# Performance work log

Hardware: AMD Instinct MI355X
Metric: run time of the kernel (lower is better)

The kernel has to match this reference:

```python
import jax, jax.numpy as jnp
import numpy as np

WS = 8          # attention window size
NUM_HEADS = 4
PATCH_RATIO = 2 # ratio between consecutive pyramid levels
SCALES = 3


def _rel_idx(ws):
    ch = np.arange(ws)
    coords = np.stack(np.meshgrid(ch, ch, indexing='ij')).reshape(2, -1)
    rel = (coords[:, :, None] - coords[:, None, :]).transpose(1, 2, 0)
    rel[:, :, 0] += ws - 1
    rel[:, :, 1] += ws - 1
    rel[:, :, 0] *= 2 * ws - 1
    return jnp.asarray(rel.sum(-1))  # [ws*ws, ws*ws] int

REL_IDX = _rel_idx(WS)


def win_part(x, ws):
    B, H, W, C = x.shape
    x = x.reshape(B, H // ws, ws, W // ws, ws, C).transpose(0, 1, 3, 2, 4, 5)
    return x.reshape(-1, ws, ws, C)


def win_rev(w, ws, B, H, W):
    C = w.shape[-1]
    x = w.reshape(B, H // ws, W // ws, ws, ws, C).transpose(0, 1, 3, 2, 4, 5)
    return x.reshape(B, H, W, C)


def cross_attn(xw, yw, mw, qw, qb, kw, kb, vw, vb, pw, pb, table):
    # xw, yw: [Bn, N, C]; mw: [Bn, N] overexposure mask
    Bn, N, C = xw.shape
    hd = C // NUM_HEADS
    scale = hd ** -0.5
    q = (xw @ qw.T + qb).reshape(Bn, N, NUM_HEADS, hd).transpose(0, 2, 1, 3) * scale
    k = (yw @ kw.T + kb).reshape(Bn, N, NUM_HEADS, hd).transpose(0, 2, 1, 3)
    v = (yw @ vw.T + vb).reshape(Bn, N, NUM_HEADS, hd).transpose(0, 2, 1, 3)
    attn = jnp.einsum('bhnd,bhmd->bhnm', q, k)
    mask_attn = mw[:, None, :] * mw[:, :, None]          # [Bn, N, N]
    attn = attn * mask_attn[:, None]                     # multiplicative exposure mask
    bias = table[REL_IDX]                                # [N, N, heads]
    attn = attn + bias.transpose(2, 0, 1)[None]
    attn = jax.nn.softmax(attn, axis=-1)
    out = jnp.einsum('bhnm,bhmd->bhnd', attn, v).transpose(0, 2, 1, 3).reshape(Bn, N, C)
    out = out @ pw.T + pb
    return out, attn


def align_level(x, y, params):
    # x, y: [B, H, W, C]; shift_size = 0 (module default)
    B, H, W, C = x.shape
    mask = jnp.where(x > 0.95, 0.0, 1.0).mean(-1, keepdims=True)  # [B,H,W,1]
    x = x * mask
    xw = win_part(x, WS).reshape(-1, WS * WS, C)
    yw = win_part(y, WS).reshape(-1, WS * WS, C)
    mw = win_part(mask, WS).reshape(-1, WS * WS)
    out, attn = cross_attn(xw, yw, mw, *params)
    out = win_rev(out.reshape(-1, WS, WS, C), WS, B, H, W)
    return out, attn


def atttransfer(ta, att, pr):
    # ta: [B, H, W, C] at finer level; att: [nW, heads, WS^2, WS^2] from coarser level
    B, H, W, C = ta.shape
    ws = WS * pr
    w = win_part(ta, ws)                                  # [nW, ws, ws, C]
    nW = w.shape[0]
    w = w.reshape(nW, WS, pr, WS, pr, C).transpose(0, 1, 3, 2, 4, 5)
    w = w.reshape(nW, WS * WS, pr * pr * C)
    out = att.mean(axis=1) @ w                            # [nW, WS^2, pr^2*C]
    out = out.reshape(nW, WS, WS, pr, pr, C).transpose(0, 1, 3, 2, 4, 5).reshape(nW, ws, ws, C)
    return win_rev(out, ws, B, H, W)


def conv3(x, w, b):
    y = jax.lax.conv_general_dilated(x, w, (1, 1), 'SAME',
                                     dimension_numbers=('NCHW', 'OIHW', 'NCHW'))
    return y + b[None, :, None, None]


def lrelu(x):
    return jax.nn.leaky_relu(x, 0.1)


def _forward(ref1, ref2, ref3, ta1, ta2, ta3, q_w, q_b, k_w, k_b, v_w, v_b,
             p_w, p_b, bias_table, fc_w, fc_b):
    refs = [ref1, ref2, ref3]
    tas = [ta1, ta2, ta3]
    upsample_feat = None
    last_att = None
    feat = None
    for i in range(SCALES, 0, -1):
        j = i - 1
        ref = refs[j].transpose(0, 2, 3, 1)   # NCHW -> NHWC
        ta = tas[j].transpose(0, 2, 3, 1)
        params = (q_w[j], q_b[j], k_w[j], k_b[j], v_w[j], v_b[j],
                  p_w[j], p_b[j], bias_table[j])
        aligned, att = align_level(ref, ta, params)
        feat = aligned.transpose(0, 3, 1, 2)  # NHWC -> NCHW
        if i < SCALES:
            atrans = atttransfer(ta, last_att, PATCH_RATIO).transpose(0, 3, 1, 2)
            feat = conv3(jnp.concatenate([feat, upsample_feat, atrans], axis=1),
                         fc_w[j], fc_b[j])
        if i > 1:
            feat = lrelu(feat)
            B, C, Hh, Ww = feat.shape
            upsample_feat = jax.image.resize(feat, (B, C, Hh * 2, Ww * 2), method='bilinear')
        last_att = att
    return lrelu(feat)


def setup_inputs() -> dict:
    key = jax.random.key(0)
    ks = jax.random.split(key, 20)
    B, C = 4, 64
    d = {}
    d['ref1'] = jax.random.normal(ks[0], (B, C, 256, 256), jnp.float32)
    d['ref2'] = jax.random.normal(ks[1], (B, C, 128, 128), jnp.float32)
    d['ref3'] = jax.random.normal(ks[2], (B, C, 64, 64), jnp.float32)
    d['ta1'] = jax.random.normal(ks[3], (B, C, 256, 256), jnp.float32)
    d['ta2'] = jax.random.normal(ks[4], (B, C, 128, 128), jnp.float32)
    d['ta3'] = jax.random.normal(ks[5], (B, C, 64, 64), jnp.float32)
    d['q_w'] = jax.random.normal(ks[6], (3, C, C), jnp.float32) * 0.02
    d['q_b'] = jax.random.normal(ks[7], (3, C), jnp.float32) * 0.02
    d['k_w'] = jax.random.normal(ks[8], (3, C, C), jnp.float32) * 0.02
    d['k_b'] = jax.random.normal(ks[9], (3, C), jnp.float32) * 0.02
    d['v_w'] = jax.random.normal(ks[10], (3, C, C), jnp.float32) * 0.02
    d['v_b'] = jax.random.normal(ks[11], (3, C), jnp.float32) * 0.02
    d['p_w'] = jax.random.normal(ks[12], (3, C, C), jnp.float32) * 0.02
    d['p_b'] = jax.random.normal(ks[13], (3, C), jnp.float32) * 0.02
    d['bias_table'] = jax.random.normal(ks[14], (3, (2 * WS - 1) ** 2, NUM_HEADS), jnp.float32) * 0.02
    d['fc_w'] = jax.random.normal(ks[15], (2, C, 3 * C, 3, 3), jnp.float32) * 0.02
    d['fc_b'] = jax.random.normal(ks[16], (2, C), jnp.float32) * 0.02
    return d


def reference(ref1, ref2, ref3, ta1, ta2, ta3, q_w, q_b, k_w, k_b, v_w, v_b,
              p_w, p_b, bias_table, fc_w, fc_b):
    return _forward(ref1, ref2, ref3, ta1, ta2, ta3, q_w, q_b, k_w, k_b,
                    v_w, v_b, p_w, p_b, bias_table, fc_w, fc_b)
```

## Files before the change

kernel.cpp:

```cpp
#include <hip/hip_runtime.h>
#include <hip/hip_bf16.h>
#include <math.h>

#define LRELU(v) ((v) >= 0.f ? (v) : 0.1f * (v))
#define LOG2E 1.4426950408889634f

typedef __attribute__((ext_vector_type(8))) short short8;
typedef __attribute__((ext_vector_type(4))) float f32x4;

#define MFMA16 __builtin_amdgcn_mfma_f32_16x16x32_bf16

__device__ __forceinline__ float loadf(const float* p) { return *p; }
__device__ __forceinline__ float loadf(const __hip_bfloat16* p) { return __bfloat162float(*p); }
__device__ __forceinline__ short f2bfbits(float f) {
    __hip_bfloat16 h = __float2bfloat16(f);
    return *reinterpret_cast<short*>(&h);
}
__device__ __forceinline__ float bits2f(unsigned short u) {
    union { unsigned int i; float f; } x; x.i = ((unsigned int)u) << 16; return x.f;
}
__device__ __forceinline__ float lo2f(unsigned int v) {
    union { unsigned int i; float f; } x; x.i = v << 16; return x.f;
}
__device__ __forceinline__ float hi2f(unsigned int v) {
    union { unsigned int i; float f; } x; x.i = v & 0xFFFF0000u; return x.f;
}

__global__ __launch_bounds__(256) void nhwc_kernel(const float* __restrict__ ref,
                                                   const float* __restrict__ ta,
                                                   __hip_bfloat16* __restrict__ refn,
                                                   __hip_bfloat16* __restrict__ tan,
                                                   float* __restrict__ maskp,
                                                   int H, int HW) {
    __shared__ float S[2][64][67];
    const int tid = threadIdx.x;
    const int tile = blockIdx.x;
    const int b = blockIdx.y;
    const int tpr = H >> 6;
    const int y = tile / tpr;
    const int x0 = (tile - y * tpr) << 6;
    const size_t ibase = (size_t)b * 64 * HW + (size_t)y * H + x0;

    for (int r = tid; r < 8192; r += 256) {
        int which = r >> 12;
        int c = (r >> 6) & 63;
        int x = r & 63;
        S[which][c][x] = (which ? ta : ref)[ibase + (size_t)c * HW + x];
    }
    __syncthreads();
    if (tid < 64) {
        float s = 0.f;
#pragma unroll
        for (int c = 0; c < 64; ++c) s += (S[0][c][tid] > 0.95f) ? 0.f : 1.f;
        maskp[(size_t)b * HW + (size_t)y * H + x0 + tid] = s * (1.f / 64.f);
    }
    const size_t obase = ((size_t)b * HW + (size_t)y * H + x0) * 64;
    for (int r = tid; r < 8192; r += 256) {
        int which = r >> 12;
        int x = (r >> 6) & 63;
        int c = r & 63;
        (which ? tan : refn)[obase + (size_t)x * 64 + c] = __float2bfloat16(S[which][c][x]);
    }
}

template <bool HASATT>
__global__ __launch_bounds__(256, 4) void fused_attn_kernel(
    const __hip_bfloat16* __restrict__ refn,
    const __hip_bfloat16* __restrict__ tan,
    const float* __restrict__ maskp,
    const __hip_bfloat16* __restrict__ WQ,
    const __hip_bfloat16* __restrict__ WK,
    const __hip_bfloat16* __restrict__ WV,
    const __hip_bfloat16* __restrict__ WPp,
    const float* __restrict__ qb, const float* __restrict__ kb,
    const float* __restrict__ vb, const float* __restrict__ pb,
    const float* __restrict__ btab,
    __hip_bfloat16* __restrict__ aligned,
    __hip_bfloat16* __restrict__ attm,
    int H, int nWx, int nWin)
{
    __shared__ __align__(16) unsigned short PP[64 * 72];
    __shared__ __align__(16) unsigned short KH[64 * 72];
    __shared__ __align__(16) unsigned short VT[64 * 72];
    __shared__ __align__(8) unsigned short BLB[900];
    __shared__ float MSK[64];

    const int HW = H * H;
    const int win = blockIdx.x;
    const int bb = blockIdx.y;
    const int wy = win / nWx, wx = win - wy * nWx;
    const int y0 = wy * 8, x0 = wx * 8;
    const int tid = threadIdx.x;
    const int w = __builtin_amdgcn_readfirstlane(tid >> 6);
    const int l = tid & 63;
    const int lq = l >> 4, lm = l & 15;

    for (int r = tid; r < 900; r += 256)
        BLB[r] = (unsigned short)f2bfbits(btab[r] * LOG2E);
    if (tid < 64)
        MSK[tid] = maskp[(size_t)bb * HW + (size_t)(y0 + (tid >> 3)) * H + x0 + (tid & 7)];

    const int tokr = 16 * w + lm;
    const size_t prow = ((size_t)bb * HW
                         + (size_t)(y0 + (tokr >> 3)) * H + (x0 + (tokr & 7))) * 64;
    const unsigned short* xp = (const unsigned short*)refn + prow;
    const unsigned short* yp = (const unsigned short*)tan + prow;

    f32x4 aq[4], ak[4], av[4];
#pragma unroll
    for (int nt = 0; nt < 4; ++nt) {
        aq[nt] = (f32x4){0.f, 0.f, 0.f, 0.f};
        ak[nt] = (f32x4){0.f, 0.f, 0.f, 0.f};
        av[nt] = (f32x4){0.f, 0.f, 0.f, 0.f};
    }

#pragma unroll
    for (int stage = 0; stage < 2; ++stage) {
        const int cio = stage * 32 + lq * 8;
        short8 xa = *reinterpret_cast<const short8*>(xp + cio);
        short8 ya = *reinterpret_cast<const short8*>(yp + cio);
#pragma unroll
        for (int nt = 0; nt < 4; ++nt) {
            const int co = nt * 16 + lm;
            short8 bq = *reinterpret_cast<const short8*>(WQ + co * 64 + cio);
            aq[nt] = MFMA16(xa, bq, aq[nt], 0, 0, 0);
            short8 bk = *reinterpret_cast<const short8*>(WK + co * 64 + cio);
            ak[nt] = MFMA16(ya, bk, ak[nt], 0, 0, 0);
            short8 bv8 = *reinterpret_cast<const short8*>(WV + co * 64 + cio);
            av[nt] = MFMA16(ya, bv8, av[nt], 0, 0, 0);
        }
    }

#pragma unroll
    for (int nt = 0; nt < 4; ++nt) {
        const int co = nt * 16 + lm;
        const float kbv = kb[co], vbv = vb[co];
#pragma unroll
        for (int r = 0; r < 4; ++r) {
            const int tr = 16 * w + lq * 4 + r;
            const int pr = 16 * (2 * (tr >> 5) + ((tr >> 2) & 1))
                         + 4 * ((tr >> 3) & 3) + (tr & 3);
            KH[pr * 72 + co] = (unsigned short)f2bfbits(ak[nt][r] + kbv);
            VT[co * 72 + tr] = (unsigned short)f2bfbits(av[nt][r] + vbv);
        }
    }
    {
        float mq_r[4];
#pragma unroll
        for (int r = 0; r < 4; ++r) mq_r[r] = MSK[16 * w + lq * 4 + r];
#pragma unroll
        for (int nt = 0; nt < 4; ++nt) {
            const float qbv = qb[nt * 16 + lm];
#pragma unroll
            for (int r = 0; r < 4; ++r)
                PP[(16 * w + lq * 4 + r) * 72 + nt * 16 + lm] =
                    (unsigned short)f2bfbits((aq[nt][r] * mq_r[r] + qbv) * 0.25f);
        }
    }
    __syncthreads();

    const short8 z8 = (short8){0, 0, 0, 0, 0, 0, 0, 0};
    const f32x4 zf = (f32x4){0.f, 0.f, 0.f, 0.f};
    short8 qfrag[4];
#pragma unroll
    for (int h = 0; h < 4; ++h)
        qfrag[h] = (lq < 2)
            ? *reinterpret_cast<const short8*>(&PP[(16 * w + lm) * 72 + 16 * h + lq * 8])
            : z8;

    const float mql = MSK[16 * w + lm] * LOG2E;
    const int qt = 16 * w + lm;
    const int qi = qt >> 3, qj = qt & 7;
    float m2[4][4];
    int bofs[4][4];
    int ktab[4][4];
#pragma unroll
    for (int nt = 0; nt < 4; ++nt)
#pragma unroll
        for (int r = 0; r < 4; ++r) {
            int kt = (nt >> 1) * 32 + lq * 8 + (nt & 1) * 4 + r;
            ktab[nt][r] = kt;
            m2[nt][r] = mql * MSK[kt];
            bofs[nt][r] = ((qi - (kt >> 3) + 7) * 15 + (qj - (kt & 7) + 7)) * 4;
        }

    float attAcc[HASATT ? 4 : 1][HASATT ? 4 : 1];
    if constexpr (HASATT) {
#pragma unroll
        for (int nt = 0; nt < 4; ++nt)
#pragma unroll
            for (int r = 0; r < 4; ++r) attAcc[nt][r] = 0.f;
    }
    f32x4 oacc[4];

#pragma unroll
    for (int hp = 0; hp < 2; ++hp) {
        unsigned int blv[4][4];
#pragma unroll
        for (int nt = 0; nt < 4; ++nt)
#pragma unroll
            for (int r = 0; r < 4; ++r)
                blv[nt][r] = *reinterpret_cast<const unsigned int*>(
                                 &BLB[bofs[nt][r] + hp * 2]);

        f32x4 s[2][4];
#pragma unroll
        for (int u = 0; u < 2; ++u) {
            const int h = hp * 2 + u;
#pragma unroll
            for (int nt = 0; nt < 4; ++nt) {
                short8 kf = (lq < 2)
                    ? *reinterpret_cast<const short8*>(
                          &KH[(nt * 16 + lm) * 72 + 16 * h + lq * 8])
                    : z8;
                s[u][nt] = MFMA16(kf, qfrag[h], zf, 0, 0, 0);
            }
        }

        float p[2][4][4];
#pragma unroll
        for (int u = 0; u < 2; ++u)
#pragma unroll
            for (int nt = 0; nt < 4; ++nt)
#pragma unroll
                for (int r = 0; r < 4; ++r) {
                    float bias = u ? hi2f(blv[nt][r]) : lo2f(blv[nt][r]);
                    p[u][nt][r] = fmaf(s[u][nt][r], m2[nt][r], bias);
                }

        float inv[2];
#pragma unroll
        for (int u = 0; u < 2; ++u) {
            float a0 = fmaxf(p[u][0][0], p[u][0][1]);
            float a1 = fmaxf(p[u][0][2], p[u][0][3]);
            float a2 = fmaxf(p[u][1][0], p[u][1][1]);
            float a3 = fmaxf(p[u][1][2], p[u][1][3]);
            float a4 = fmaxf(p[u][2][0], p[u][2][1]);
            float a5 = fmaxf(p[u][2][2], p[u][2][3]);
            float a6 = fmaxf(p[u][3][0], p[u][3][1]);
            float a7 = fmaxf(p[u][3][2], p[u][3][3]);
            float b0 = fmaxf(a0, a1), b1 = fmaxf(a2, a3);
            float b2 = fmaxf(a4, a5), b3 = fmaxf(a6, a7);
            float m = fmaxf(fmaxf(b0, b1), fmaxf(b2, b3));
            m = fmaxf(m, __shfl_xor(m, 16));
            m = fmaxf(m, __shfl_xor(m, 32));
            float sm = 0.f;
#pragma unroll
            for (int nt = 0; nt < 4; ++nt)
#pragma unroll
                for (int r = 0; r < 4; ++r) {
                    p[u][nt][r] = exp2f(p[u][nt][r] - m);
                    sm += p[u][nt][r];
                }
            sm += __shfl_xor(sm, 16);
            sm += __shfl_xor(sm, 32);
            inv[u] = 1.f / sm;
        }

        if constexpr (HASATT) {
#pragma unroll
            for (int u = 0; u < 2; ++u) {
                const float sc = 0.25f * inv[u];
#pragma unroll
                for (int nt = 0; nt < 4; ++nt)
#pragma unroll
                    for (int r = 0; r < 4; ++r)
                        attAcc[nt][r] = fmaf(sc, p[u][nt][r], attAcc[nt][r]);
            }
        }

#pragma unroll
        for (int u = 0; u < 2; ++u) {
            const int h = hp * 2 + u;
            short8 pb0, pb1;
#pragma unroll
            for (int j = 0; j < 8; ++j) {
                pb0[j] = f2bfbits(p[u][(j >> 2)][j & 3]);
                pb1[j] = f2bfbits(p[u][2 + (j >> 2)][j & 3]);
            }
            short8 vt0 = *reinterpret_cast<const short8*>(&VT[(16 * h + lm) * 72 + lq * 8]);
            short8 vt1 = *reinterpret_cast<const short8*>(&VT[(16 * h + lm) * 72 + 32 + lq * 8]);
            f32x4 o = MFMA16(vt0, pb0, zf, 0, 0, 0);
            o = MFMA16(vt1, pb1, o, 0, 0, 0);
            oacc[h][0] = o[0] * inv[u]; oacc[h][1] = o[1] * inv[u];
            oacc[h][2] = o[2] * inv[u]; oacc[h][3] = o[3] * inv[u];
        }
    }

    if constexpr (HASATT) {
#pragma unroll
        for (int nt = 0; nt < 4; ++nt)
#pragma unroll
            for (int r = 0; r < 4; ++r)
                PP[(16 * w + lm) * 72 + ktab[nt][r]] =
                    (unsigned short)f2bfbits(attAcc[nt][r]);
        const int rr = 16 * w + (l >> 2), cb = (l & 3) * 16;
        short8 a0 = *reinterpret_cast<const short8*>(&PP[rr * 72 + cb]);
        short8 a1 = *reinterpret_cast<const short8*>(&PP[rr * 72 + cb + 8]);
        unsigned short* gp = (unsigned short*)attm
            + ((size_t)bb * nWin + win) * 4096 + (size_t)rr * 64 + cb;
        *reinterpret_cast<short8*>(gp) = a0;
        *reinterpret_cast<short8*>(gp + 8) = a1;
    }

    short8 oa0, oa1;
#pragma unroll
    for (int j = 0; j < 8; ++j) {
        oa0[j] = f2bfbits(oacc[(j >> 2)][j & 3]);
        oa1[j] = f2bfbits(oacc[2 + (j >> 2)][j & 3]);
    }
    f32x4 eo[4];
#pragma unroll
    for (int nt = 0; nt < 4; ++nt) {
        const int co = nt * 16 + lm;
        short8 wb0 = *reinterpret_cast<const short8*>(WPp + co * 64 + lq * 8);
        short8 wb1 = *reinterpret_cast<const short8*>(WPp + co * 64 + 32 + lq * 8);
        eo[nt] = MFMA16(oa0, wb0, zf, 0, 0, 0);
        eo[nt] = MFMA16(oa1, wb1, eo[nt], 0, 0, 0);
    }
    const size_t obase = (size_t)bb * HW * 64;
#pragma unroll
    for (int nt = 0; nt < 4; ++nt) {
        float pbv = pb[nt * 16 + lm];
#pragma unroll
        for (int r = 0; r < 4; ++r) {
            int tok = 16 * w + lq * 4 + r;
            aligned[obase + ((size_t)(y0 + (tok >> 3)) * H + (x0 + (tok & 7))) * 64
                    + nt * 16 + lm] = __float2bfloat16(eo[nt][r] + pbv);
        }
    }
}

__global__ __launch_bounds__(256) void wsplit_kernel(const float* __restrict__ qw,
                                                     const float* __restrict__ kw,
                                                     const float* __restrict__ vw,
                                                     const float* __restrict__ pw,
                                                     __hip_bfloat16* __restrict__ dst) {
    int idx = blockIdx.x * 256 + threadIdx.x;
    int e = idx & 4095;
    int mat = (idx >> 12) & 3;
    int j = idx >> 14;
    int co = e >> 6, ci = e & 63;
    int src_ci = ci;
    if (mat == 3)
        src_ci = 16 * (2 * (ci >> 5) + ((ci >> 2) & 1)) + 4 * ((ci >> 3) & 3) + (ci & 3);
    const float* src = (mat == 0 ? qw : mat == 1 ? kw : mat == 2 ? vw : pw) + j * 4096;
    float v = src[co * 64 + src_ci];
    __hip_bfloat16 h = __float2bfloat16(v);
    dst[((size_t)j * 4 + mat) * 8192 + e] = h;
    dst[((size_t)j * 4 + mat) * 8192 + 4096 + e] = __float2bfloat16(v - __bfloat162float(h));
}

#define PSTR 4624
__global__ __launch_bounds__(256) void atttrans_kernel(
    const __hip_bfloat16* __restrict__ tan,
    const __hip_bfloat16* __restrict__ attm,
    __hip_bfloat16* __restrict__ outw,
    int H, int HW, int nWx16)
{
    __shared__ __align__(16) unsigned short AT[4608];
    __shared__ __align__(16) unsigned short VTP[4 * PSTR];

    const int tid = threadIdx.x;
    const int win = blockIdx.x;
    const int b = blockIdx.y;
    const int wh = win / nWx16, ww = win - wh * nWx16;
    const int w = __builtin_amdgcn_readfirstlane(tid >> 6);
    const int l = tid & 63;
    const int lq = l >> 4, lm = l & 15;

    const unsigned short* ap = (const unsigned short*)attm
        + ((size_t)b * nWx16 * nWx16 + win) * 4096;
    for (int s = tid; s < 512; s += 256) {
        short8 v = *reinterpret_cast<const short8*>(ap + s * 8);
        *reinterpret_cast<short8*>(&AT[(s >> 3) * 72 + (s & 7) * 8]) = v;
    }

    {
        const int yy = tid >> 4, xx = tid & 15;
        const int pp = ((yy & 1) << 1) | (xx & 1);
        const int s = ((yy >> 1) << 3) | (xx >> 1);
        const unsigned short* tp = (const unsigned short*)tan
            + ((size_t)b * HW + (size_t)(wh * 16 + yy) * H + (ww * 16 + xx)) * 64;
        unsigned short* vbp = &VTP[pp * PSTR + s];
#pragma unroll
        for (int oct = 0; oct < 8; ++oct) {
            short8 v = *reinterpret_cast<const short8*>(tp + oct * 8);
#pragma unroll
            for (int i = 0; i < 8; ++i) vbp[(oct * 8 + i) * 72] = (unsigned short)v[i];
        }
    }
    __syncthreads();

    f32x4 acc[4][4];
#pragma unroll
    for (int pp = 0; pp < 4; ++pp)
#pragma unroll
        for (int nt = 0; nt < 4; ++nt) acc[pp][nt] = (f32x4){0.f, 0.f, 0.f, 0.f};

#pragma unroll
    for (int kk = 0; kk < 2; ++kk) {
        short8 aA = *reinterpret_cast<const short8*>(
                        &AT[(16 * w + lm) * 72 + kk * 32 + lq * 8]);
#pragma unroll
        for (int pp = 0; pp < 4; ++pp) {
#pragma unroll
            for (int nt = 0; nt < 4; ++nt) {
                short8 bB = *reinterpret_cast<const short8*>(
                    &VTP[pp * PSTR + (nt * 16 + lm) * 72 + kk * 32 + lq * 8]);
                acc[pp][nt] = MFMA16(aA, bB, acc[pp][nt], 0, 0, 0);
            }
        }
    }

#pragma unroll
    for (int pp = 0; pp < 4; ++pp) {
        const int pi = pp >> 1, pj = pp & 1;
#pragma unroll
        for (int r = 0; r < 4; ++r) {
            const int t = 16 * w + lq * 4 + r;
            const int Y = wh * 16 + ((t >> 3) << 1) + pi;
            const int X = ww * 16 + ((t & 7) << 1) + pj;
            __hip_bfloat16* op = outw + ((size_t)b * HW + (size_t)Y * H + X) * 64;
#pragma unroll
            for (int nt = 0; nt < 4; ++nt)
                op[nt * 16 + lm] = __float2bfloat16(acc[pp][nt][r]);
        }
    }
}

__global__ __launch_bounds__(256) void wtrans_kernel(const float* __restrict__ src,
                                                     __hip_bfloat16* __restrict__ WH,
                                                     __hip_bfloat16* __restrict__ WL) {
    int idx = blockIdx.x * 256 + threadIdx.x;
    int j = idx & 7;
    int t1 = idx >> 3;
    int co = t1 & 63;
    int t2 = t1 >> 6;
    int oct = t2 & 3;
    int t3 = t2 >> 2;
    int chunk = t3 % 6;
    int kykx = t3 / 6;
    int ci = chunk * 32 + oct * 8 + j;
    int ky = kykx / 3, kx = kykx % 3;
    float v = src[((co * 192 + ci) * 3 + ky) * 3 + kx];
    __hip_bfloat16 h = __float2bfloat16(v);
    WH[idx] = h;
    WL[idx] = __float2bfloat16(v - __bfloat162float(h));
}

__global__ __launch_bounds__(256) void conv_mfma_kernel(
    const __hip_bfloat16* __restrict__ s0, const __hip_bfloat16* __restrict__ s1,
    const __hip_bfloat16* __restrict__ s2,
    const __hip_bfloat16* __restrict__ WHp,
    const float* __restrict__ bias,
    float* __restrict__ out,
    int H, int HW, int mode)
{
    __shared__ short I[6][66][40];

    const int tid = threadIdx.x;
    const int w   = tid >> 6;
    const int l   = tid & 63;
    const int lq  = l >> 4;
    const int lm  = l & 15;
    const int x0  = blockIdx.x * 64;
    const int y0  = blockIdx.y * 4;
    const size_t zoff = (size_t)blockIdx.z * HW * 64;
    const short8 z8 = (short8){0, 0, 0, 0, 0, 0, 0, 0};

    f32x4 acc[4][4];
#pragma unroll
    for (int mt = 0; mt < 4; ++mt)
#pragma unroll
        for (int nt = 0; nt < 4; ++nt) acc[mt][nt] = (f32x4){0.f, 0.f, 0.f, 0.f};

    const short8* WH8 = reinterpret_cast<const short8*>(WHp);

    short8 st[7];
    const unsigned short* b0 = (const unsigned short*)s0;
    const unsigned short* b1 = (const unsigned short*)s1;
    const unsigned short* b2 = (const unsigned short*)s2;

    auto stage_load = [&](int chunk) {
        const unsigned short* src = (chunk < 2) ? b0 : (chunk < 4) ? b1 : b2;
        const int cib = (chunk & 1) * 32;
#pragma unroll
        for (int s = 0; s < 7; ++s) {
            int slot = tid + (s << 8);
            if (slot < 1584) {
                int oct = slot & 3;
                int xr = slot >> 2;
                int xi = xr % 66;
                int r = xr / 66;
                int gx = x0 - 1 + xi, gy = y0 - 1 + r;
                short8 v = z8;
                if (gx >= 0 && gx < H && gy >= 0 && gy < H)
                    v = *reinterpret_cast<const short8*>(
                            src + zoff + ((size_t)gy * H + gx) * 64 + cib + oct * 8);
                st[s] = v;
            }
        }
    };
    auto stage_write = [&]() {
#pragma unroll
        for (int s = 0; s < 7; ++s) {
            int slot = tid + (s << 8);
            if (slot < 1584) {
                int oct = slot & 3;
                int xr = slot >> 2;
                int xi = xr % 66;
                int r = xr / 66;
                *reinterpret_cast<short8*>(&I[r][xi][oct * 8]) = st[s];
            }
        }
    };

    stage_load(0);
    stage_write();
    __syncthreads();

    for (int chunk = 0; chunk < 6; ++chunk) {
        if (chunk < 5) stage_load(chunk + 1);
#pragma unroll
        for (int kk = 0; kk < 9; ++kk) {
            const int ky = kk / 3, kx = kk % 3;
            const int wbase = ((kk * 6 + chunk) * 4 + lq) * 64 + lm;
            short8 ah[4];
#pragma unroll
            for (int mt = 0; mt < 4; ++mt) ah[mt] = WH8[wbase + mt * 16];
#pragma unroll
            for (int nt = 0; nt < 4; ++nt) {
                short8 bfrag = *reinterpret_cast<const short8*>(
                                   &I[w + ky][nt * 16 + lm + kx][lq * 8]);
#pragma unroll
                for (int mt = 0; mt < 4; ++mt)
                    acc[mt][nt] = MFMA16(ah[mt], bfrag, acc[mt][nt], 0, 0, 0);
            }
        }
        if (chunk < 5) {
            __syncthreads();
            stage_write();
            __syncthreads();
        }
    }

    const int y = y0 + w;
#pragma unroll
    for (int mt = 0; mt < 4; ++mt) {
#pragma unroll
        for (int r = 0; r < 4; ++r) {
            const int co = mt * 16 + lq * 4 + r;
            const float bv = bias[co];
#pragma unroll
            for (int nt = 0; nt < 4; ++nt) {
                float v = acc[mt][nt][r] + bv;
                const int x = x0 + nt * 16 + lm;
                if (mode == 0) {
                    v = LRELU(v);
                    out[zoff + (size_t)co * HW + (size_t)y * H + x] = v;
                } else {
                    out[zoff + ((size_t)y * H + x) * 64 + co] = v;
                }
            }
        }
    }
}

template <typename T>
__global__ __launch_bounds__(256) void upsample_kernel(const T* __restrict__ in,
                                                       __hip_bfloat16* __restrict__ out,
                                                       int Hin, int total) {
    int idx = blockIdx.x * 256 + threadIdx.x;
    if (idx >= total) return;
    int c = idx & 63;
    int r1 = idx >> 6;
    int W2 = Hin * 2;
    int X = r1 % W2;
    int r2 = r1 / W2;
    int Y = r2 % W2;
    int b = r2 / W2;
    int y0 = Y >> 1, x0 = X >> 1;
    int ya = (Y & 1) ? y0 + 1 : y0 - 1;
    int xa = (X & 1) ? x0 + 1 : x0 - 1;
    ya = ya < 0 ? 0 : (ya >= Hin ? Hin - 1 : ya);
    xa = xa < 0 ? 0 : (xa >= Hin ? Hin - 1 : xa);
    const T* p = in + (size_t)b * Hin * Hin * 64;
    float v00 = LRELU(loadf(p + ((size_t)y0 * Hin + x0) * 64 + c));
    float v01 = LRELU(loadf(p + ((size_t)y0 * Hin + xa) * 64 + c));
    float v10 = LRELU(loadf(p + ((size_t)ya * Hin + x0) * 64 + c));
    float v11 = LRELU(loadf(p + ((size_t)ya * Hin + xa) * 64 + c));
    out[idx] = __float2bfloat16(0.5625f * v00 + 0.1875f * (v01 + v10) + 0.0625f * v11);
}

extern "C" void kernel_launch(void* const* d_in, const int* in_sizes, int n_in,
                              void* d_out, int out_size, void* d_ws, size_t ws_size,
                              hipStream_t stream) {
    const float* refs[3] = { (const float*)d_in[0], (const float*)d_in[1], (const float*)d_in[2] };
    const float* tas[3]  = { (const float*)d_in[3], (const float*)d_in[4], (const float*)d_in[5] };
    const float* q_w = (const float*)d_in[6];
    const float* q_b = (const float*)d_in[7];
    const float* k_w = (const float*)d_in[8];
    const float* k_b = (const float*)d_in[9];
    const float* v_w = (const float*)d_in[10];
    const float* v_b = (const float*)d_in[11];
    const float* p_w = (const float*)d_in[12];
    const float* p_b = (const float*)d_in[13];
    const float* btab = (const float*)d_in[14];
    const float* fc_w = (const float*)d_in[15];
    const float* fc_b = (const float*)d_in[16];

    const size_t WBYTES = 4ull * 221184 + 196608;
    const size_t BIG4 = 4ull * 65536 * 64 * 2;
    const size_t NEED4 = WBYTES + 4 * BIG4 + 4ull * 65536 * 4 + 4096;
    const int NB = (ws_size >= NEED4) ? 4 : 1;
    const size_t BIG = (size_t)NB * 65536 * 64 * 2;

    char* p = (char*)d_ws;
    __hip_bfloat16* WH0 = (__hip_bfloat16*)p;  p += 221184;
    __hip_bfloat16* WL0 = (__hip_bfloat16*)p;  p += 221184;
    __hip_bfloat16* WH1 = (__hip_bfloat16*)p;  p += 221184;
    __hip_bfloat16* WL1 = (__hip_bfloat16*)p;  p += 221184;
    __hip_bfloat16* WTA = (__hip_bfloat16*)p;  p += 196608;
    __hip_bfloat16* XRN = (__hip_bfloat16*)p;  p += BIG;
    __hip_bfloat16* XTN = (__hip_bfloat16*)p;  p += BIG;
    __hip_bfloat16* ALIGNED = (__hip_bfloat16*)p;  p += BIG;
    __hip_bfloat16* UPS     = (__hip_bfloat16*)p;  p += BIG;
    float* MASKP = (float*)p;  p += (size_t)NB * 65536 * 4;
    __hip_bfloat16* ATRANS = XRN;
    __hip_bfloat16 *ATTMA, *ATTMB;
    float* FEAT2;
    if (NB == 4) {
        ATTMA = (__hip_bfloat16*)d_out;
        ATTMB = (__hip_bfloat16*)((float*)d_out + 1048576);
        FEAT2 = (float*)d_out + 5242880;
    } else {
        ATTMA = (__hip_bfloat16*)p;  p += (size_t)64 * 4096 * 2;
        ATTMB = (__hip_bfloat16*)p;  p += (size_t)256 * 4096 * 2;
        FEAT2 = (float*)p;           p += (size_t)16384 * 64 * 4;
    }

    wtrans_kernel<<<432, 256, 0, stream>>>(fc_w, WH0, WL0);
    wtrans_kernel<<<432, 256, 0, stream>>>(fc_w + 110592, WH1, WL1);
    wsplit_kernel<<<192, 256, 0, stream>>>(q_w, k_w, v_w, p_w, WTA);

    for (int b0 = 0; b0 < 4; b0 += NB) {
        const float* ref1 = refs[0] + (size_t)b0 * 64 * 65536;
        const float* ta1  = tas[0]  + (size_t)b0 * 64 * 65536;
        const float* ref2 = refs[1] + (size_t)b0 * 64 * 16384;
        const float* ta2  = tas[1]  + (size_t)b0 * 64 * 16384;
        const float* ref3 = refs[2] + (size_t)b0 * 64 * 4096;
        const float* ta3  = tas[2]  + (size_t)b0 * 64 * 4096;

        nhwc_kernel<<<dim3(64, NB), 256, 0, stream>>>(ref3, ta3, XRN, XTN, MASKP, 64, 4096);
        fused_attn_kernel<true><<<dim3(64, NB), 256, 0, stream>>>(
            XRN, XTN, MASKP,
            WTA + (2*4+0)*8192, WTA + (2*4+1)*8192, WTA + (2*4+2)*8192, WTA + (2*4+3)*8192,
            q_b + 2*64, k_b + 2*64, v_b + 2*64, p_b + 2*64,
            btab + 2*900, ALIGNED, ATTMA, 64, 8, 64);
        upsample_kernel<__hip_bfloat16><<<(NB * 64 * 16384) / 256, 256, 0, stream>>>(
            ALIGNED, UPS, 64, NB * 64 * 16384);

        nhwc_kernel<<<dim3(256, NB), 256, 0, stream>>>(ref2, ta2, XRN, XTN, MASKP, 128, 16384);
        fused_attn_kernel<true><<<dim3(256, NB), 256, 0, stream>>>(
            XRN, XTN, MASKP,
            WTA + (1*4+0)*8192, WTA + (1*4+1)*8192, WTA + (1*4+2)*8192, WTA + (1*4+3)*8192,
            q_b + 64, k_b + 64, v_b + 64, p_b + 64,
            btab + 900, ALIGNED, ATTMB, 128, 16, 256);
        atttrans_kernel<<<dim3(64, NB), 256, 0, stream>>>(
            XTN, ATTMA, ATRANS, 128, 16384, 8);
        conv_mfma_kernel<<<dim3(2, 32, NB), 256, 0, stream>>>(
            ALIGNED, UPS, ATRANS, WH1, fc_b + 64, FEAT2, 128, 16384, 1);
        upsample_kernel<float><<<(NB * 64 * 65536) / 256, 256, 0, stream>>>(
            FEAT2, UPS, 128, NB * 64 * 65536);

        nhwc_kernel<<<dim3(1024, NB), 256, 0, stream>>>(ref1, ta1, XRN, XTN, MASKP, 256, 65536);
        fused_attn_kernel<false><<<dim3(1024, NB), 256, 0, stream>>>(
            XRN, XTN, MASKP,
            WTA + 0*8192, WTA + 1*8192, WTA + 2*8192, WTA + 3*8192,
            q_b, k_b, v_b, p_b,
            btab, ALIGNED, nullptr, 256, 32, 1024);
        atttrans_kernel<<<dim3(256, NB), 256, 0, stream>>>(
            XTN, ATTMB, ATRANS, 256, 65536, 16);
        conv_mfma_kernel<<<dim3(4, 64, NB), 256, 0, stream>>>(
            ALIGNED, UPS, ATRANS, WH0, fc_b,
            (float*)d_out + (size_t)b0 * 64 * 65536, 256, 65536, 0);
    }
}
```

Baseline: 411.2 us.

## Load conv input fragments directly from global memory instead of LDS staging

Removes the shared-memory tile, its register-staged double buffering, and the block barriers in the 3x3 conv MFMA kernel. Each lane now reads its B-fragment straight from global memory, with bounds checks for the padding. This drops the LDS traffic and synchronisation. In exchange, each input element is re-fetched up to nine times (3x3 taps) across waves and relies on the caches to absorb it, and global-load latency is no longer hidden by the prefetch pipeline.

```diff
diff --git a/kernel.cpp b/kernel.cpp
--- a/kernel.cpp
+++ b/kernel.cpp
@@ -457,8 +457,6 @@
     float* __restrict__ out,
     int H, int HW, int mode)
 {
-    __shared__ short I[6][66][40];
-
     const int tid = threadIdx.x;
     const int w   = tid >> 6;
     const int l   = tid & 63;
@@ -476,52 +474,13 @@
         for (int nt = 0; nt < 4; ++nt) acc[mt][nt] = (f32x4){0.f, 0.f, 0.f, 0.f};
 
     const short8* WH8 = reinterpret_cast<const short8*>(WHp);
-
-    short8 st[7];
-    const unsigned short* b0 = (const unsigned short*)s0;
-    const unsigned short* b1 = (const unsigned short*)s1;
-    const unsigned short* b2 = (const unsigned short*)s2;
-
-    auto stage_load = [&](int chunk) {
-        const unsigned short* src = (chunk < 2) ? b0 : (chunk < 4) ? b1 : b2;
-        const int cib = (chunk & 1) * 32;
-#pragma unroll
-        for (int s = 0; s < 7; ++s) {
-            int slot = tid + (s << 8);
-            if (slot < 1584) {
-                int oct = slot & 3;
-                int xr = slot >> 2;
-                int xi = xr % 66;
-                int r = xr / 66;
-                int gx = x0 - 1 + xi, gy = y0 - 1 + r;
-                short8 v = z8;
-                if (gx >= 0 && gx < H && gy >= 0 && gy < H)
-                    v = *reinterpret_cast<const short8*>(
-                            src + zoff + ((size_t)gy * H + gx) * 64 + cib + oct * 8);
-                st[s] = v;
-            }
-        }
-    };
-    auto stage_write = [&]() {
-#pragma unroll
-        for (int s = 0; s < 7; ++s) {
-            int slot = tid + (s << 8);
-            if (slot < 1584) {
-                int oct = slot & 3;
-                int xr = slot >> 2;
-                int xi = xr % 66;
-                int r = xr / 66;
-                *reinterpret_cast<short8*>(&I[r][xi][oct * 8]) = st[s];
-            }
-        }
-    };
-
-    stage_load(0);
-    stage_write();
-    __syncthreads();
+    const unsigned short* bases[3] = { (const unsigned short*)s0,
+                                       (const unsigned short*)s1,
+                                       (const unsigned short*)s2 };
 
     for (int chunk = 0; chunk < 6; ++chunk) {
-        if (chunk < 5) stage_load(chunk + 1);
+        const unsigned short* src = bases[chunk >> 1];
+        const int cio = (chunk & 1) * 32 + lq * 8;
 #pragma unroll
         for (int kk = 0; kk < 9; ++kk) {
             const int ky = kk / 3, kx = kk % 3;
@@ -529,19 +488,19 @@
             short8 ah[4];
 #pragma unroll
             for (int mt = 0; mt < 4; ++mt) ah[mt] = WH8[wbase + mt * 16];
+            const int gy = y0 + w + ky - 1;
+            const bool rowok = (gy >= 0) && (gy < H);
 #pragma unroll
             for (int nt = 0; nt < 4; ++nt) {
-                short8 bfrag = *reinterpret_cast<const short8*>(
-                                   &I[w + ky][nt * 16 + lm + kx][lq * 8]);
+                const int gx = x0 + nt * 16 + lm + kx - 1;
+                short8 bfrag = z8;
+                if (rowok && gx >= 0 && gx < H)
+                    bfrag = *reinterpret_cast<const short8*>(
+                                src + zoff + ((size_t)gy * H + gx) * 64 + cio);
 #pragma unroll
                 for (int mt = 0; mt < 4; ++mt)
                     acc[mt][nt] = MFMA16(ah[mt], bfrag, acc[mt][nt], 0, 0, 0);
             }
-        }
-        if (chunk < 5) {
-            __syncthreads();
-            stage_write();
-            __syncthreads();
         }
     }
 
```

Result: slower. 497.2 us (+20.9%).
